# Kernel optimization log

Measured on AMD Instinct MI355X. Metric: run time of the kernel, lower is better.

Reference implementation:

```python
import math
import jax, jax.numpy as jnp
import numpy as np

C_S, C_Z = 384, 128
H, D = 12, 16           # heads, head dim
PQ, PV = 4, 8           # query / value points
INF, EPS = 100000.0, 1e-8
OUT_IN = H * D + H * PV * 4 + H * C_Z  # 2112


def setup_inputs() -> dict:
    key = jax.random.key(0)
    ks = jax.random.split(key, 20)
    B, N = 2, 512
    def tn(k, shape, fan_in):
        # truncated-normal-ish init, std = sqrt(1/fan_in)
        return jax.random.truncated_normal(k, -2.0, 2.0, shape, jnp.float32) * math.sqrt(1.0 / fan_in)
    inp = {
        'single_representation': jax.random.normal(ks[0], (B, N, C_S), jnp.float32),
        'pair_representation': jax.random.normal(ks[1], (B, N, N, C_Z), jnp.float32),
        'rotations': jax.random.normal(ks[2], (B, N, 3, 3), jnp.float32),
        'translation': jax.random.normal(ks[3], (B, N, 3), jnp.float32),
        'seq_mask': jnp.ones((B, N), jnp.float32),
        # weights stored as [in, out] (i.e. torch weight transposed)
        'wq': tn(ks[4], (C_S, H * D), C_S), 'bq': jnp.zeros((H * D,), jnp.float32),
        'wkv': tn(ks[5], (C_S, 2 * H * D), C_S), 'bkv': jnp.zeros((2 * H * D,), jnp.float32),
        'wqp': tn(ks[6], (C_S, 3 * H * PQ), C_S), 'bqp': jnp.zeros((3 * H * PQ,), jnp.float32),
        'wkvp': tn(ks[7], (C_S, 3 * H * (PQ + PV)), C_S), 'bkvp': jnp.zeros((3 * H * (PQ + PV),), jnp.float32),
        'wb': tn(ks[8], (C_Z, H), C_Z), 'bb': jnp.zeros((H,), jnp.float32),
        # original uses 'final' (zero) init; use small random so output/grads are nontrivial
        'wout': tn(ks[9], (OUT_IN, C_S), OUT_IN) * 0.1, 'bout': jnp.zeros((C_S,), jnp.float32),
        'head_weights': jax.random.normal(ks[10], (H,), jnp.float32) * 0.1,
    }
    return inp


def _project_points(s, w, b, P):
    raw = s @ w + b                             # [B,N,3*H*P]
    x, y, z = jnp.split(raw, 3, axis=-1)
    pts = jnp.stack([x, y, z], axis=-1)         # [B,N,H*P,3]
    B, N = s.shape[0], s.shape[1]
    return pts.reshape(B, N, H, P, 3)


def ipa_forward(single_representation, pair_representation, rotations, translation, seq_mask,
                wq, bq, wkv, bkv, wqp, bqp, wkvp, bkvp, wb, bb, wout, bout, head_weights):
    s, z, R, t, m = single_representation, pair_representation, rotations, translation, seq_mask
    B, N = s.shape[0], s.shape[1]
    q = (s @ wq + bq).reshape(B, N, H, D)
    kv = (s @ wkv + bkv).reshape(B, N, H, 2 * D)
    k, v = jnp.split(kv, 2, axis=-1)
    qp = _project_points(s, wqp, bqp, PQ)
    kvp = _project_points(s, wkvp, bkvp, PQ + PV)
    kp, vp = kvp[..., :PQ, :], kvp[..., PQ:, :]
    to_glob = lambda p: jnp.einsum('biop,bihqp->bihqo', R, p) + t[:, :, None, None, :]
    qg, kg, vg = to_glob(qp), to_glob(kp), to_glob(vp)
    bias = z @ wb + bb                          # [B,N,N,H]
    logits = jnp.einsum('bihd,bjhd->bhij', q, k) * math.sqrt(1.0 / (3.0 * D))
    logits = logits + math.sqrt(1.0 / 3.0) * jnp.transpose(bias, (0, 3, 1, 2))
    diff = qg[:, :, None] - kg[:, None]         # [B,Ni,Nj,H,PQ,3]
    pa = jnp.sum(diff * diff, axis=-1)          # [B,Ni,Nj,H,PQ]
    hw = jax.nn.softplus(head_weights).reshape(1, 1, 1, H, 1) * math.sqrt(1.0 / (3.0 * (PQ * 9.0 / 2.0)))
    pa = jnp.sum(pa * hw, axis=-1) * (-0.5)     # [B,Ni,Nj,H]
    logits = logits + jnp.transpose(pa, (0, 3, 1, 2))
    sq_mask = m[:, :, None] * m[:, None, :]
    logits = logits + INF * (sq_mask[:, None] - 1.0)
    attn = jax.nn.softmax(logits, axis=-1)      # [B,H,Ni,Nj]
    out_scalar = jnp.einsum('bhij,bjhd->bihd', attn, v).reshape(B, N, H * D)
    rpg = jnp.einsum('bhij,bjhqc->bihqc', attn, vg)
    rpl = jnp.einsum('biop,bihqp->bihqo', jnp.swapaxes(R, -1, -2), rpg - t[:, :, None, None, :])
    norms = jnp.sqrt(jnp.sum(rpl * rpl, axis=-1) + EPS).reshape(B, N, H * PV)
    rpl = rpl.reshape(B, N, H * PV, 3)
    out_pair = jnp.einsum('bhij,bijd->bihd', attn, z).reshape(B, N, H * C_Z)
    feats = jnp.concatenate([out_scalar, rpl[..., 0], rpl[..., 1], rpl[..., 2], norms, out_pair], axis=-1)
    out = feats @ wout + bout
    return out * m[:, :, None]


def reference(single_representation, pair_representation, rotations, translation, seq_mask,
              wq, bq, wkv, bkv, wqp, bqp, wkvp, bkvp, wb, bb, wout, bout, head_weights):
    return ipa_forward(single_representation, pair_representation, rotations, translation, seq_mask,
                       wq, bq, wkv, bkv, wqp, bqp, wkvp, bkvp, wb, bb, wout, bout, head_weights)
```

## Files before the change

### kernel.cpp

```cpp
#include <hip/hip_runtime.h>


typedef __attribute__((ext_vector_type(8))) short bf16x8;
typedef __attribute__((ext_vector_type(4))) float f32x4;
typedef __attribute__((ext_vector_type(4))) unsigned int u32x4;
typedef __attribute__((ext_vector_type(2))) unsigned int u32x2;

__device__ __forceinline__ unsigned short f2b(float f) {
  union { float f; unsigned int u; } x; x.f = f;
  unsigned int r = (x.u + 0x7FFFu + ((x.u >> 16) & 1u)) >> 16;
  return (unsigned short)r;
}
__device__ __forceinline__ float b2f(unsigned short u) {
  return __builtin_bit_cast(float, (unsigned int)u << 16);
}
__device__ __forceinline__ unsigned int cvtpk(float lo, float hi) {
  unsigned int r;
  asm("v_cvt_pk_bf16_f32 %0, %1, %2" : "=v"(r) : "v"(lo), "v"(hi));
  return r;
}
__device__ __forceinline__ int zaddrc(int c, int j) {
  return (((c << 8) + (j << 1)) ^ ((c & 7) << 4) ^ (((c >> 3) & 7) << 5));
}
__device__ __forceinline__ float wsrc(const float* wq, const float* wkv,
                                      const float* wqp, const float* wkvp, int k, int o) {
  if (o < 192)  return wq[k * 192 + o];
  if (o < 576)  return wkv[k * 384 + (o - 192)];
  if (o < 720)  return wqp[k * 144 + (o - 576)];
  return wkvp[k * 432 + (o - 720)];
}
__device__ __forceinline__ float bsrc(const float* bq, const float* bkv,
                                      const float* bqp, const float* bkvp, int o) {
  if (o < 192)  return bq[o];
  if (o < 576)  return bkv[o - 192];
  if (o < 720)  return bqp[o - 576];
  return bkvp[o - 720];
}

__global__ __launch_bounds__(256) void k_prep(
    const float* __restrict__ wout, unsigned short* __restrict__ woutT,
    const float* __restrict__ wq, const float* __restrict__ wkv,
    const float* __restrict__ wqp, const float* __restrict__ wkvp,
    unsigned short* __restrict__ WT) {
  __shared__ float tile[32][33];
  int tid = threadIdx.x;
  int tx = tid & 31, ty = tid >> 5;
  if (blockIdx.x < 792) {
    int bx = blockIdx.x;
    int kb = (bx % 66) * 32, cb = (bx / 66) * 32;
    #pragma unroll
    for (int r = ty; r < 32; r += 8) tile[r][tx] = wout[(size_t)(kb + r) * 384 + cb + tx];
    __syncthreads();
    #pragma unroll
    for (int r = ty; r < 32; r += 8) woutT[(size_t)(cb + r) * 2112 + kb + tx] = f2b(tile[tx][r]);
  } else {
    int bx = blockIdx.x - 792;
    int kb = (bx % 12) * 32, ob = (bx / 12) * 32;
    #pragma unroll
    for (int r = ty; r < 32; r += 8) tile[r][tx] = wsrc(wq, wkv, wqp, wkvp, kb + r, ob + tx);
    __syncthreads();
    #pragma unroll
    for (int r = ty; r < 32; r += 8) WT[(size_t)(ob + r) * 384 + kb + tx] = f2b(tile[tx][r]);
  }
}

__global__ __launch_bounds__(256) void k_projG(
    const float* __restrict__ s, const unsigned short* __restrict__ WT,
    const float* __restrict__ bq, const float* __restrict__ bkv,
    const float* __restrict__ bqp, const float* __restrict__ bkvp,
    float* __restrict__ qws,
    unsigned short* __restrict__ kb2, unsigned short* __restrict__ vT,
    float* __restrict__ rawp) {
  int tid = threadIdx.x;
  int wv = tid >> 6, l = tid & 63, lr = l & 15, lk = l >> 4;
  int wm = wv >> 1, wn = wv & 1;
  int i0 = blockIdx.x * 64, o0 = blockIdx.y * 64;
  f32x4 acc[2][2] = {};

  #pragma unroll 3
  for (int ks = 0; ks < 12; ks++) {
    int k0 = ks * 32;
    bf16x8 af[2], bf[2];
    #pragma unroll
    for (int mf = 0; mf < 2; mf++) {
      int i = i0 + wm * 32 + mf * 16 + lr;
      const float4* sp = (const float4*)(s + (size_t)i * 384 + k0);
      float4 a0 = sp[lk * 2], a1 = sp[lk * 2 + 1];
      u32x4 afp;
      afp[0] = cvtpk(a0.x, a0.y); afp[1] = cvtpk(a0.z, a0.w);
      afp[2] = cvtpk(a1.x, a1.y); afp[3] = cvtpk(a1.z, a1.w);
      af[mf] = __builtin_bit_cast(bf16x8, afp);
    }
    #pragma unroll
    for (int nf = 0; nf < 2; nf++) {
      int o = o0 + wn * 32 + nf * 16 + lr;
      bf[nf] = *(const bf16x8*)(WT + (size_t)o * 384 + k0 + lk * 8);
    }
    #pragma unroll
    for (int mf = 0; mf < 2; mf++)
      #pragma unroll
      for (int nf = 0; nf < 2; nf++)
        acc[mf][nf] = __builtin_amdgcn_mfma_f32_16x16x32_bf16(af[mf], bf[nf], acc[mf][nf], 0, 0, 0);
  }

  #pragma unroll
  for (int mf = 0; mf < 2; mf++) {
    #pragma unroll
    for (int nf = 0; nf < 2; nf++) {
      int o = o0 + wn * 32 + nf * 16 + lr;
      float bias = bsrc(bq, bkv, bqp, bkvp, o);
      #pragma unroll
      for (int reg = 0; reg < 4; reg++) {
        int i = i0 + wm * 32 + mf * 16 + lk * 4 + reg;
        float v = acc[mf][nf][reg] + bias;
        int b2 = i >> 9, jj = i & 511;
        if (o < 192) {
          qws[(size_t)i * 192 + o] = v;
        } else if (o < 576) {
          int c = o - 192, h = c >> 5, e = c & 31;
          if (e < 16)
            kb2[(((size_t)b2 * 12 + h) * 512 + jj) * 40 + e] = f2b(v);
          else
            vT[((size_t)b2 * 480 + h * 16 + (e - 16)) * 512 + jj] = f2b(v);
        } else {
          rawp[(size_t)i * 576 + (o - 576)] = v;
        }
      }
    }
  }
}

__global__ __launch_bounds__(512) void k_points(
    const float* __restrict__ rawp,
    const float* __restrict__ rot, const float* __restrict__ trn,
    const float* __restrict__ hwt,
    float* __restrict__ qgws, float* __restrict__ qnws,
    unsigned short* __restrict__ kb2, unsigned short* __restrict__ vT) {
  __shared__ float praw[4][576];
  int tid = threadIdx.x;
  int row0 = blockIdx.x * 4;

  for (int idx = tid; idx < 2304; idx += 512)
    praw[idx / 576][idx % 576] = rawp[(size_t)row0 * 576 + idx];
  __syncthreads();

  for (int idx = tid; idx < 768; idx += 512) {
    int r = idx / 192, p = idx % 192;
    int bi = row0 + r;
    int bb2 = bi >> 9, jj = bi & 511;
    const float* Rm = rot + (size_t)bi * 9;
    const float* tv = trn + (size_t)bi * 3;
    float x, y, z;
    if (p < 48) { x = praw[r][p]; y = praw[r][48 + p]; z = praw[r][96 + p]; }
    else { int q = p - 48; x = praw[r][144 + q]; y = praw[r][288 + q]; z = praw[r][432 + q]; }
    float gx = Rm[0] * x + Rm[1] * y + Rm[2] * z + tv[0];
    float gy = Rm[3] * x + Rm[4] * y + Rm[5] * z + tv[1];
    float gz = Rm[6] * x + Rm[7] * y + Rm[8] * z + tv[2];
    if (p < 48) {
      float* dst = qgws + (size_t)bi * 144 + p * 3;
      dst[0] = gx; dst[1] = gy; dst[2] = gz;
    } else {
      int q12 = p - 48; int h = q12 / 12, qq = q12 % 12;
      if (qq < 4) {
        size_t base = (((size_t)bb2 * 12 + h) * 512 + jj) * 40 + 16 + qq * 3;
        kb2[base + 0] = f2b(gx); kb2[base + 1] = f2b(gy); kb2[base + 2] = f2b(gz);
      } else {
        size_t base = ((size_t)bb2 * 480 + 192 + h * 24 + (qq - 4) * 3) * 512 + jj;
        vT[base] = f2b(gx); vT[base + 512] = f2b(gy); vT[base + 1024] = f2b(gz);
      }
    }
  }

  if (tid < 48) {
    int r = tid / 12, h = tid % 12;
    int bi = row0 + r;
    int bb2 = bi >> 9, jj = bi & 511;
    const float* Rm = rot + (size_t)bi * 9;
    const float* tv = trn + (size_t)bi * 3;
    float hw = 0.5f * logf(1.0f + __expf(hwt[h])) * 0.13608276348795434f;
    float qn = 0.f, kn = 0.f;
    #pragma unroll
    for (int qq = 0; qq < 4; qq++) {
      {
        int p = h * 4 + qq;
        float x = praw[r][p], y = praw[r][48 + p], z = praw[r][96 + p];
        float gx = Rm[0]*x + Rm[1]*y + Rm[2]*z + tv[0];
        float gy = Rm[3]*x + Rm[4]*y + Rm[5]*z + tv[1];
        float gz = Rm[6]*x + Rm[7]*y + Rm[8]*z + tv[2];
        qn += gx*gx + gy*gy + gz*gz;
      }
      {
        int q = h * 12 + qq;
        float x = praw[r][144 + q], y = praw[r][288 + q], z = praw[r][432 + q];
        float gx = Rm[0]*x + Rm[1]*y + Rm[2]*z + tv[0];
        float gy = Rm[3]*x + Rm[4]*y + Rm[5]*z + tv[1];
        float gz = Rm[6]*x + Rm[7]*y + Rm[8]*z + tv[2];
        kn += gx*gx + gy*gy + gz*gz;
      }
    }
    qnws[(size_t)bi * 12 + h] = qn;
    float pr = -hw * kn;
    unsigned short hi = f2b(pr);
    unsigned short lo = f2b(pr - b2f(hi));
    size_t base = (((size_t)bb2 * 12 + h) * 512 + jj) * 40;
    kb2[base + 28] = hi; kb2[base + 29] = lo;
    kb2[base + 30] = 0x3F80; kb2[base + 31] = 0x3F80;
  }
}

__global__ __launch_bounds__(256) void k_qkpa(
    const float* __restrict__ qws, const float* __restrict__ qgws,
    const float* __restrict__ qnws, const float* __restrict__ hwt,
    const float* __restrict__ mrow,
    const unsigned short* __restrict__ kb2,
    float* __restrict__ qkpa) {
  __shared__ unsigned short aq[64 * 40];
  __shared__ float mI[64];
  __shared__ float mJ[512];
  int bh = blockIdx.x;
  int b = bh / 12, h = bh - b * 12;
  int i0 = blockIdx.y * 64;
  int tid = threadIdx.x;
  float hw = 0.5f * logf(1.0f + __expf(hwt[h])) * 0.13608276348795434f;

  for (int idx = tid; idx < 512; idx += 256) mJ[idx] = mrow[b * 512 + idx];
  if (tid < 64) mI[tid] = mrow[b * 512 + i0 + tid];
  {
    int r = tid >> 2, c0 = (tid & 3) * 10;
    size_t gi = (size_t)b * 512 + i0 + r;
    const float* qr = qws + gi * 192 + h * 16;
    const float* gr = qgws + gi * 144 + h * 12;
    float pr = -hw * qnws[gi * 12 + h];
    unsigned short hi = f2b(pr);
    unsigned short lo = f2b(pr - b2f(hi));
    for (int c = c0; c < c0 + 10; c++) {
      unsigned short v;
      if (c < 16)      v = f2b(0.14433756729740643f * qr[c]);
      else if (c < 28) v = f2b(2.0f * hw * gr[c - 16]);
      else if (c < 30) v = 0x3F80;
      else if (c == 30) v = hi;
      else              v = lo;
      aq[r * 40 + c] = v;
    }
  }
  __syncthreads();

  int w = tid >> 6, l = tid & 63, lr = l & 15, lk = l >> 4;
  int n0 = w * 128;
  bf16x8 afr[4];
  #pragma unroll
  for (int mf = 0; mf < 4; mf++)
    afr[mf] = *(const bf16x8*)&aq[(mf * 16 + lr) * 40 + lk * 8];
  const unsigned short* kbb = kb2 + (size_t)bh * 512 * 40;
  #pragma unroll 2
  for (int nf = 0; nf < 8; nf++) {
    int j = n0 + nf * 16 + lr;
    float mjv = mJ[j];
    bf16x8 bfr = *(const bf16x8*)(kbb + (size_t)j * 40 + lk * 8);
    #pragma unroll
    for (int mf = 0; mf < 4; mf++) {
      f32x4 acc = {0.f, 0.f, 0.f, 0.f};
      acc = __builtin_amdgcn_mfma_f32_16x16x32_bf16(afr[mf], bfr, acc, 0, 0, 0);
      #pragma unroll
      for (int r = 0; r < 4; r++) {
        int il = mf * 16 + lk * 4 + r;
        int i = i0 + il;
        float val = acc[r] + 100000.0f * (mI[il] * mjv - 1.0f);
        qkpa[((size_t)(b * 512 + i) * 12 + h) * 512 + j] = val;
      }
    }
  }
}

__global__ __launch_bounds__(512, 2) void k_attn(
    const float* __restrict__ z,
    const float* __restrict__ wb, const float* __restrict__ bb,
    const float* __restrict__ qkpa,
    unsigned short* __restrict__ attnG,
    unsigned short* __restrict__ feats) {
  __shared__ __align__(16) char zbfc[32768];
  __shared__ __align__(16) unsigned short attnbF[8192];
  __shared__ __align__(16) float logitsC[12][132];
  __shared__ unsigned short wbT[2048];
  __shared__ float bbl[16];
  __shared__ float mrun[12], lrun[12], frh[16], m_used[12][4], rinv[16];

  int tid = threadIdx.x;
  int bi = blockIdx.x;
  int b = bi >> 9;
  const float* zbase = z + (size_t)bi * 65536;
  int wv = tid >> 6, l = tid & 63, lr = l & 15, lk = l >> 4;

  if (tid < 16) bbl[tid] = (tid < 12) ? bb[tid] : 0.0f;
  else if (tid >= 16 && tid < 28) { mrun[tid - 16] = -1e30f; lrun[tid - 16] = 0.f; }
  else if (tid >= 28 && tid < 44) frh[tid - 28] = 1.0f;
  for (int idx = tid; idx < 2048; idx += 512) {
    int h = idx >> 7, c = idx & 127;
    wbT[h * 128 + c] = (h < 12) ? f2b(wb[c * 12 + h]) : (unsigned short)0;
  }
  __syncthreads();

  bf16x8 bfrag[4];
  #pragma unroll
  for (int kc = 0; kc < 4; kc++)
    bfrag[kc] = *(const bf16x8*)(wbT + lr * 128 + kc * 32 + lk * 8);

  f32x4 accPC = {0.f, 0.f, 0.f, 0.f};
  int c0 = wv * 16;

  #pragma unroll 1
  for (int ch = 0; ch < 4; ch++) {
    int j0 = ch * 128;
    {
      int jl = wv * 16 + lr;
      const float4* zp = (const float4*)(zbase + (size_t)(j0 + jl) * 128);
      float4 zr[8];
      #pragma unroll
      for (int q = 0; q < 8; q++) zr[q] = zp[(q >> 1) * 8 + lk * 2 + (q & 1)];
      f32x4 acc = {0.f, 0.f, 0.f, 0.f};
      #pragma unroll
      for (int kc = 0; kc < 4; kc++) {
        float4 a0 = zr[kc * 2], a1 = zr[kc * 2 + 1];
        unsigned int p0 = cvtpk(a0.x, a0.y), p1 = cvtpk(a0.z, a0.w);
        unsigned int p2 = cvtpk(a1.x, a1.y), p3 = cvtpk(a1.z, a1.w);
        u32x4 af = {p0, p1, p2, p3};
        acc = __builtin_amdgcn_mfma_f32_16x16x32_bf16(__builtin_bit_cast(bf16x8, af), bfrag[kc], acc, 0, 0, 0);
        int cb = kc * 32 + lk * 8;
        unsigned int pv[4] = {p0, p1, p2, p3};
        #pragma unroll
        for (int m = 0; m < 4; m++) {
          int cc = cb + 2 * m;
          *(unsigned short*)(zbfc + zaddrc(cc, jl))     = (unsigned short)(pv[m] & 0xffffu);
          *(unsigned short*)(zbfc + zaddrc(cc + 1, jl)) = (unsigned short)(pv[m] >> 16);
        }
      }
      if (lr < 12) {
        #pragma unroll
        for (int reg = 0; reg < 4; reg++)
          logitsC[lr][wv * 16 + lk * 4 + reg] = 0.5773502691896258f * (acc[reg] + bbl[lr]);
      }
    }
    __syncthreads();

    if (tid < 384) {
      int h = tid >> 5, g = tid & 31;
      float4 v = *(const float4*)&logitsC[h][g * 4];
      float4 q4 = *(const float4*)(qkpa + (size_t)bi * 6144 + h * 512 + j0 + g * 4);
      v.x += q4.x; v.y += q4.y; v.z += q4.z; v.w += q4.w;
      float pmx = fmaxf(fmaxf(v.x, v.y), fmaxf(v.z, v.w));
      #pragma unroll
      for (int off = 16; off > 0; off >>= 1) pmx = fmaxf(pmx, __shfl_xor(pmx, off, 32));
      float m_old = mrun[h];
      float m_new = fmaxf(m_old, pmx);
      float fr = __expf(m_old - m_new);
      float4 e;
      e.x = __expf(v.x - m_new); e.y = __expf(v.y - m_new);
      e.z = __expf(v.z - m_new); e.w = __expf(v.w - m_new);
      float s = e.x + e.y + e.z + e.w;
      #pragma unroll
      for (int off = 16; off > 0; off >>= 1) s += __shfl_xor(s, off, 32);
      if (g == 0) {
        lrun[h] = lrun[h] * fr + s;
        mrun[h] = m_new;
        m_used[h][ch] = m_new;
        frh[h] = fr;
      }
      u32x2 ob;
      ob[0] = cvtpk(e.x, e.y); ob[1] = cvtpk(e.z, e.w);
      int j4 = j0 + g * 4;
      int byte = (h * 1024 + j4 * 2) ^ ((h & 7) << 4);
      *(u32x2*)((char*)attnbF + byte) = ob;
    }
    __syncthreads();

    {
      float fr = frh[lr];
      accPC[0] *= fr; accPC[1] *= fr; accPC[2] *= fr; accPC[3] *= fr;
      int arow = c0 + lr;
      #pragma unroll
      for (int jt = 0; jt < 4; jt++) {
        int jbl = jt * 32 + lk * 8;
        bf16x8 afrag = *(const bf16x8*)(zbfc + zaddrc(arow, jbl));
        int pb = (lr * 1024 + (j0 + jbl) * 2) ^ ((lr & 7) << 4);
        bf16x8 pfrag = *(const bf16x8*)((const char*)attnbF + pb);
        accPC = __builtin_amdgcn_mfma_f32_16x16x32_bf16(afrag, pfrag, accPC, 0, 0, 0);
      }
    }
    __syncthreads();
  }

  if (tid < 16) rinv[tid] = (tid < 12) ? (1.0f / lrun[tid]) : 0.0f;
  __syncthreads();

  size_t fb = (size_t)bi * 2112;

  if (tid < 384) {
    int h = tid >> 5, g = tid & 31;
    float rn = rinv[h];
    float mf = mrun[h];
    unsigned short* gout = attnG + (((size_t)(b * 12 + h) * 512) + (bi & 511)) * 512;
    #pragma unroll
    for (int ch = 0; ch < 4; ch++) {
      float sc = __expf(m_used[h][ch] - mf) * rn;
      int j4 = ch * 128 + g * 4;
      int byte = (h * 1024 + j4 * 2) ^ ((h & 7) << 4);
      u32x2 ob = *(const u32x2*)((const char*)attnbF + byte);
      float f0 = b2f((unsigned short)(ob[0] & 0xffffu)) * sc;
      float f1 = b2f((unsigned short)(ob[0] >> 16)) * sc;
      float f2 = b2f((unsigned short)(ob[1] & 0xffffu)) * sc;
      float f3 = b2f((unsigned short)(ob[1] >> 16)) * sc;
      u32x2 ow;
      ow[0] = cvtpk(f0, f1); ow[1] = cvtpk(f2, f3);
      *(u32x2*)(gout + j4) = ow;
    }
  }

  if (lr < 12) {
    float rn = rinv[lr];
    u32x2 ow;
    ow[0] = cvtpk(accPC[0] * rn, accPC[1] * rn);
    ow[1] = cvtpk(accPC[2] * rn, accPC[3] * rn);
    *(u32x2*)&feats[fb + 576 + lr * 128 + c0 + lk * 4] = ow;
  }
}

__global__ __launch_bounds__(256) void k_av(
    const unsigned short* __restrict__ attnG, const unsigned short* __restrict__ vT,
    const float* __restrict__ rot, const float* __restrict__ trn,
    unsigned short* __restrict__ feats) {
  __shared__ float sc[64 * 24];
  __shared__ float rotL[64 * 9];
  __shared__ float trnL[64 * 3];
  int bh = blockIdx.x;
  int b = bh / 12, h = bh - b * 12;
  int i0 = blockIdx.y * 64;
  int tid = threadIdx.x;

  for (int idx = tid; idx < 576; idx += 256) rotL[idx] = rot[((size_t)b * 512 + i0) * 9 + idx];
  for (int idx = tid; idx < 192; idx += 256) trnL[idx] = trn[((size_t)b * 512 + i0) * 3 + idx];

  int w = tid >> 6, l = tid & 63, lr = l & 15, lk = l >> 4;
  int iw = w * 16;
  const unsigned short* Abase = attnG + ((size_t)bh * 512 + i0 + iw) * 512;
  const unsigned short* vTb = vT + (size_t)b * 480 * 512;
  int cm[3];
  #pragma unroll
  for (int nf = 0; nf < 3; nf++) {
    int c = nf * 16 + lr;
    cm[nf] = (c < 16) ? (h * 16 + c) : (c < 40 ? 192 + h * 24 + (c - 16) : 0);
  }
  f32x4 acc[3] = {};
  #pragma unroll 2
  for (int jb = 0; jb < 512; jb += 32) {
    bf16x8 a0 = *(const bf16x8*)(Abase + (size_t)lr * 512 + jb + lk * 8);
    #pragma unroll
    for (int nf = 0; nf < 3; nf++) {
      bf16x8 bfr = *(const bf16x8*)(vTb + (size_t)cm[nf] * 512 + jb + lk * 8);
      acc[nf] = __builtin_amdgcn_mfma_f32_16x16x32_bf16(a0, bfr, acc[nf], 0, 0, 0);
    }
  }
  #pragma unroll
  for (int nf = 0; nf < 3; nf++) {
    int c = nf * 16 + lr;
    #pragma unroll
    for (int r = 0; r < 4; r++) {
      int il = iw + lk * 4 + r;
      float v = acc[nf][r];
      if (c < 16) feats[(size_t)(b * 512 + i0 + il) * 2112 + h * 16 + c] = f2b(v);
      else if (c < 40) sc[il * 24 + (c - 16)] = v;
    }
  }
  __syncthreads();
  #pragma unroll
  for (int k2 = 0; k2 < 2; k2++) {
    int itm = tid + k2 * 256;
    int il = itm >> 3, pv = itm & 7;
    float gx = sc[il * 24 + pv * 3 + 0] - trnL[il * 3 + 0];
    float gy = sc[il * 24 + pv * 3 + 1] - trnL[il * 3 + 1];
    float gz = sc[il * 24 + pv * 3 + 2] - trnL[il * 3 + 2];
    const float* R = &rotL[il * 9];
    float lx = R[0] * gx + R[3] * gy + R[6] * gz;
    float ly = R[1] * gx + R[4] * gy + R[7] * gz;
    float lz = R[2] * gx + R[5] * gy + R[8] * gz;
    size_t fb = (size_t)(b * 512 + i0 + il) * 2112;
    feats[fb + 192 + h * 8 + pv] = f2b(lx);
    feats[fb + 288 + h * 8 + pv] = f2b(ly);
    feats[fb + 384 + h * 8 + pv] = f2b(lz);
    feats[fb + 480 + h * 8 + pv] = f2b(sqrtf(lx * lx + ly * ly + lz * lz + 1e-8f));
  }
}

__global__ __launch_bounds__(256) void k_out(const unsigned short* __restrict__ feats,
                                             const unsigned short* __restrict__ woutT,
                                             const float* __restrict__ bout,
                                             const float* __restrict__ mrow,
                                             float* __restrict__ out) {
  __shared__ unsigned short At[2048];
  __shared__ unsigned short Bt[1024];
  int m0 = blockIdx.x * 64, n0 = blockIdx.y * 32;
  int tid = threadIdx.x;
  int wv = tid >> 6, l = tid & 63, lr = l & 15, lk = l >> 4;
  int wm = wv >> 1, wn = wv & 1;
  f32x4 acc[2] = {};
  int sr = tid >> 2, sq = tid & 3;
  const char* fbase = (const char*)feats + (size_t)(m0 + sr) * 4224 + sq * 16;
  int swA = (sr * 64 + sq * 16) ^ ((sr & 7) << 4);
  int rb = tid >> 2, qb = tid & 3;
  const char* bbase = (const char*)woutT + (size_t)(n0 + rb) * 4224 + qb * 16;
  int swB = (rb * 64 + qb * 16) ^ ((rb & 7) << 4);

  uint4 av = *(const uint4*)(fbase);
  uint4 bv = {0, 0, 0, 0};
  if (tid < 128) bv = *(const uint4*)(bbase);
  for (int k0 = 0; k0 < 2112; k0 += 32) {
    __syncthreads();
    *(uint4*)((char*)At + swA) = av;
    if (tid < 128) *(uint4*)((char*)Bt + swB) = bv;
    __syncthreads();
    if (k0 + 32 < 2112) {
      av = *(const uint4*)(fbase + (size_t)(k0 + 32) * 2);
      if (tid < 128) bv = *(const uint4*)(bbase + (size_t)(k0 + 32) * 2);
    }
    bf16x8 af[2], bfv;
    #pragma unroll
    for (int mt = 0; mt < 2; mt++) {
      int row = wm * 32 + mt * 16 + lr;
      af[mt] = *(const bf16x8*)((const char*)At + ((row * 64 + lk * 16) ^ ((row & 7) << 4)));
    }
    {
      int row = wn * 16 + lr;
      bfv = *(const bf16x8*)((const char*)Bt + ((row * 64 + lk * 16) ^ ((row & 7) << 4)));
    }
    #pragma unroll
    for (int mt = 0; mt < 2; mt++)
      acc[mt] = __builtin_amdgcn_mfma_f32_16x16x32_bf16(af[mt], bfv, acc[mt], 0, 0, 0);
  }

  #pragma unroll
  for (int mt = 0; mt < 2; mt++) {
    int nc = n0 + wn * 16 + lr;
    float bo = bout[nc];
    #pragma unroll
    for (int reg = 0; reg < 4; reg++) {
      int rowg = m0 + wm * 32 + mt * 16 + lk * 4 + reg;
      out[(size_t)rowg * 384 + nc] = (acc[mt][reg] + bo) * mrow[rowg];
    }
  }
}

extern "C" void kernel_launch(void* const* d_in, const int* in_sizes, int n_in,
                              void* d_out, int out_size, void* d_ws, size_t ws_size,
                              hipStream_t stream) {
  const float* s    = (const float*)d_in[0];
  const float* z    = (const float*)d_in[1];
  const float* rot  = (const float*)d_in[2];
  const float* trn  = (const float*)d_in[3];
  const float* msk  = (const float*)d_in[4];
  const float* wq   = (const float*)d_in[5];
  const float* bq   = (const float*)d_in[6];
  const float* wkv  = (const float*)d_in[7];
  const float* bkv  = (const float*)d_in[8];
  const float* wqp  = (const float*)d_in[9];
  const float* bqp  = (const float*)d_in[10];
  const float* wkvp = (const float*)d_in[11];
  const float* bkvp = (const float*)d_in[12];
  const float* wb   = (const float*)d_in[13];
  const float* bb   = (const float*)d_in[14];
  const float* wout = (const float*)d_in[15];
  const float* bout = (const float*)d_in[16];
  const float* hwt  = (const float*)d_in[17];

  float* qws  = (float*)d_ws;
  float* qgws = qws + 196608;
  float* qnws = qgws + 147456;
  float* qkpa = qnws + 12288;
  float* rawp = qkpa + 6291456;
  unsigned short* vT    = (unsigned short*)(rawp + 589824);
  unsigned short* kb2   = vT + 491520;
  unsigned short* attnG = kb2 + 491520;
  unsigned short* feats = attnG + 6291456;
  unsigned short* woutT = feats + 2162688;
  unsigned short* WT    = woutT + 811008;
  float* out = (float*)d_out;

  k_prep<<<dim3(1224), dim3(256), 0, stream>>>(wout, woutT, wq, wkv, wqp, wkvp, WT);
  k_projG<<<dim3(16, 18), dim3(256), 0, stream>>>(s, WT, bq, bkv, bqp, bkvp,
                                                  qws, kb2, vT, rawp);
  k_points<<<dim3(256), dim3(512), 0, stream>>>(rawp, rot, trn, hwt, qgws, qnws, kb2, vT);
  k_qkpa<<<dim3(24, 8), dim3(256), 0, stream>>>(qws, qgws, qnws, hwt, msk, kb2, qkpa);
  k_attn<<<dim3(1024), dim3(512), 0, stream>>>(z, wb, bb, qkpa, attnG, feats);
  k_av<<<dim3(24, 8), dim3(256), 0, stream>>>(attnG, vT, rot, trn, feats);
  k_out<<<dim3(16, 12), dim3(256), 0, stream>>>(feats, woutT, bout, msk, out);
}
```

Baseline: 139.8 us.

## Stage fp32 pair tiles in LDS via direct global-to-LDS loads in k_attn

The attention kernel now streams each 128-row chunk of the pair representation straight from global memory into a swizzled fp32 LDS buffer using global_load_lds. It drops the per-thread register loads and the scalar bf16 transposed stores. Both the bias projection and the attn·z product read from this buffer and convert to bf16 on the fly. LDS use roughly doubles, so launch bounds drop to one block per CU. This trades occupancy and extra LDS read and convert work for lower VGPR and store pressure.

Measured after the change: 158.6 us (median of 2 runs). 1.13x slower.

```diff
diff --git a/kernel.cpp b/kernel.cpp
--- a/kernel.cpp
+++ b/kernel.cpp
@@ -19,8 +19,10 @@
   asm("v_cvt_pk_bf16_f32 %0, %1, %2" : "=v"(r) : "v"(lo), "v"(hi));
   return r;
 }
-__device__ __forceinline__ int zaddrc(int c, int j) {
-  return (((c << 8) + (j << 1)) ^ ((c & 7) << 4) ^ (((c >> 3) & 7) << 5));
+__device__ __forceinline__ void gload_lds16(const void* g, void* l) {
+  __builtin_amdgcn_global_load_lds(
+      (const __attribute__((address_space(1))) void*)g,
+      (__attribute__((address_space(3))) void*)l, 16, 0, 0);
 }
 __device__ __forceinline__ float wsrc(const float* wq, const float* wkv,
                                       const float* wqp, const float* wkvp, int k, int o) {
@@ -272,67 +274,71 @@
   }
 }
 
-__global__ __launch_bounds__(512, 2) void k_attn(
+__global__ __launch_bounds__(512, 1) void k_attn(
     const float* __restrict__ z,
     const float* __restrict__ wb, const float* __restrict__ bb,
     const float* __restrict__ qkpa,
     unsigned short* __restrict__ attnG,
     unsigned short* __restrict__ feats) {
-  __shared__ __align__(16) char zbfc[32768];
-  __shared__ __align__(16) unsigned short attnbF[8192];
+  __shared__ __align__(16) char zf32c[65536];
+  __shared__ __align__(16) unsigned short attnbF[6144];
   __shared__ __align__(16) float logitsC[12][132];
-  __shared__ unsigned short wbT[2048];
+  __shared__ unsigned short wbT[1536];
   __shared__ float bbl[16];
   __shared__ float mrun[12], lrun[12], frh[16], m_used[12][4], rinv[16];
 
   int tid = threadIdx.x;
   int bi = blockIdx.x;
   int b = bi >> 9;
-  const float* zbase = z + (size_t)bi * 65536;
+  const char* zbaseB = (const char*)(z + (size_t)bi * 65536);
   int wv = tid >> 6, l = tid & 63, lr = l & 15, lk = l >> 4;
 
   if (tid < 16) bbl[tid] = (tid < 12) ? bb[tid] : 0.0f;
   else if (tid >= 16 && tid < 28) { mrun[tid - 16] = -1e30f; lrun[tid - 16] = 0.f; }
   else if (tid >= 28 && tid < 44) frh[tid - 28] = 1.0f;
-  for (int idx = tid; idx < 2048; idx += 512) {
+  for (int idx = tid; idx < 1536; idx += 512) {
     int h = idx >> 7, c = idx & 127;
-    wbT[h * 128 + c] = (h < 12) ? f2b(wb[c * 12 + h]) : (unsigned short)0;
+    wbT[h * 128 + c] = f2b(wb[c * 12 + h]);
   }
   __syncthreads();
 
+  int hcl = (lr < 12) ? lr : 0;
   bf16x8 bfrag[4];
   #pragma unroll
   for (int kc = 0; kc < 4; kc++)
-    bfrag[kc] = *(const bf16x8*)(wbT + lr * 128 + kc * 32 + lk * 8);
+    bfrag[kc] = *(const bf16x8*)(wbT + hcl * 128 + kc * 32 + lk * 8);
 
   f32x4 accPC = {0.f, 0.f, 0.f, 0.f};
   int c0 = wv * 16;
+  int ldsbase = wv * 1024 + l * 16;
 
   #pragma unroll 1
   for (int ch = 0; ch < 4; ch++) {
     int j0 = ch * 128;
     {
-      int jl = wv * 16 + lr;
-      const float4* zp = (const float4*)(zbase + (size_t)(j0 + jl) * 128);
-      float4 zr[8];
-      #pragma unroll
-      for (int q = 0; q < 8; q++) zr[q] = zp[(q >> 1) * 8 + lk * 2 + (q & 1)];
+      const char* gchunk = zbaseB + (size_t)j0 * 512;
+      #pragma unroll
+      for (int q = 0; q < 8; q++) {
+        int L = q * 8192 + ldsbase;
+        int src = L ^ (((L >> 9) & 7) << 4);
+        gload_lds16(gchunk + src, zf32c + (q * 8192 + wv * 1024));
+      }
+    }
+    __syncthreads();
+
+    {
+      int jb = wv * 16 + lr;
+      int sw = (jb & 7) << 4;
       f32x4 acc = {0.f, 0.f, 0.f, 0.f};
       #pragma unroll
       for (int kc = 0; kc < 4; kc++) {
-        float4 a0 = zr[kc * 2], a1 = zr[kc * 2 + 1];
-        unsigned int p0 = cvtpk(a0.x, a0.y), p1 = cvtpk(a0.z, a0.w);
-        unsigned int p2 = cvtpk(a1.x, a1.y), p3 = cvtpk(a1.z, a1.w);
-        u32x4 af = {p0, p1, p2, p3};
+        int bbyte = jb * 512 + (kc * 32 + lk * 8) * 4;
+        float4 a0 = *(const float4*)(zf32c + (bbyte ^ sw));
+        float4 a1 = *(const float4*)(zf32c + ((bbyte + 16) ^ sw));
+        u32x4 af;
+        af[0] = cvtpk(a0.x, a0.y); af[1] = cvtpk(a0.z, a0.w);
+        af[2] = cvtpk(a1.x, a1.y); af[3] = cvtpk(a1.z, a1.w);
         acc = __builtin_amdgcn_mfma_f32_16x16x32_bf16(__builtin_bit_cast(bf16x8, af), bfrag[kc], acc, 0, 0, 0);
-        int cb = kc * 32 + lk * 8;
-        unsigned int pv[4] = {p0, p1, p2, p3};
-        #pragma unroll
-        for (int m = 0; m < 4; m++) {
-          int cc = cb + 2 * m;
-          *(unsigned short*)(zbfc + zaddrc(cc, jl))     = (unsigned short)(pv[m] & 0xffffu);
-          *(unsigned short*)(zbfc + zaddrc(cc + 1, jl)) = (unsigned short)(pv[m] >> 16);
-        }
       }
       if (lr < 12) {
         #pragma unroll
@@ -356,11 +362,11 @@
       float4 e;
       e.x = __expf(v.x - m_new); e.y = __expf(v.y - m_new);
       e.z = __expf(v.z - m_new); e.w = __expf(v.w - m_new);
-      float s = e.x + e.y + e.z + e.w;
-      #pragma unroll
-      for (int off = 16; off > 0; off >>= 1) s += __shfl_xor(s, off, 32);
+      float sm = e.x + e.y + e.z + e.w;
+      #pragma unroll
+      for (int off = 16; off > 0; off >>= 1) sm += __shfl_xor(sm, off, 32);
       if (g == 0) {
-        lrun[h] = lrun[h] * fr + s;
+        lrun[h] = lrun[h] * fr + sm;
         mrun[h] = m_new;
         m_used[h][ch] = m_new;
         frh[h] = fr;
@@ -374,16 +380,22 @@
     __syncthreads();
 
     {
-      float fr = frh[lr];
+      float fr = frh[hcl];
       accPC[0] *= fr; accPC[1] *= fr; accPC[2] *= fr; accPC[3] *= fr;
-      int arow = c0 + lr;
       #pragma unroll
       for (int jt = 0; jt < 4; jt++) {
-        int jbl = jt * 32 + lk * 8;
-        bf16x8 afrag = *(const bf16x8*)(zbfc + zaddrc(arow, jbl));
-        int pb = (lr * 1024 + (j0 + jbl) * 2) ^ ((lr & 7) << 4);
+        u32x4 afp;
+        #pragma unroll
+        for (int e2 = 0; e2 < 4; e2++) {
+          int ja = jt * 32 + lk * 8 + e2 * 2;
+          int jb2 = ja + 1;
+          float f1 = *(const float*)(zf32c + ((ja * 512 + (c0 + lr) * 4) ^ ((ja & 7) << 4)));
+          float f2 = *(const float*)(zf32c + ((jb2 * 512 + (c0 + lr) * 4) ^ ((jb2 & 7) << 4)));
+          afp[e2] = cvtpk(f1, f2);
+        }
+        int pb = (hcl * 1024 + (j0 + jt * 32 + lk * 8) * 2) ^ ((hcl & 7) << 4);
         bf16x8 pfrag = *(const bf16x8*)((const char*)attnbF + pb);
-        accPC = __builtin_amdgcn_mfma_f32_16x16x32_bf16(afrag, pfrag, accPC, 0, 0, 0);
+        accPC = __builtin_amdgcn_mfma_f32_16x16x32_bf16(__builtin_bit_cast(bf16x8, afp), pfrag, accPC, 0, 0, 0);
       }
     }
     __syncthreads();
```
